# Kernel optimization log

Measured on AMD Instinct MI355X. Metric: run time of the kernel, lower is better.

## Reference

```python
import jax, jax.numpy as jnp
import numpy as np

SIGMA_MIN, SIGMA_MAX = 0.03, 0.35
LAMBDA_GEO = 8.0
COMPAT_SCALE = 0.1
INVALID_W = 0.05
NH, HD = 8, 64
LN_EPS = 1e-5

def _ln(x, g, b):
    m = x.mean(-1, keepdims=True)
    v = ((x - m) ** 2).mean(-1, keepdims=True)
    return (x - m) * jax.lax.rsqrt(v + LN_EPS) * g + b

def setup_inputs() -> dict:
    key = jax.random.key(0)
    ks = jax.random.split(key, 32)
    B, C, H, W = 8, 512, 32, 32
    T, S, D, SIN = 1024, 1024, 512, 512
    s = 0.02
    inp = {
        'front_feat': jax.random.normal(ks[0], (B, C, H, W), jnp.float32),
        'sat_tokens': jax.random.normal(ks[1], (B, S, SIN), jnp.float32),
        'sat_xy': jax.random.uniform(ks[2], (B, S, 2), jnp.float32),
        'front_bev_xy': jax.random.uniform(ks[3], (B, T, 2), jnp.float32),
        'front_bev_valid_mask': jax.random.bernoulli(ks[4], 0.9, (B, T)),
        'front_plucker': jax.random.normal(ks[5], (B, T, 6), jnp.float32),
        'fa_w': jax.random.normal(ks[6], (C, D), jnp.float32) * s,
        'fa_b': jnp.zeros((D,), jnp.float32),
        'fa_g': jnp.ones((D,), jnp.float32),
        'fa_lb': jnp.zeros((D,), jnp.float32),
        'sa_w': jax.random.normal(ks[7], (SIN, D), jnp.float32) * s,
        'sa_b': jnp.zeros((D,), jnp.float32),
        'sa_g': jnp.ones((D,), jnp.float32),
        'sa_lb': jnp.zeros((D,), jnp.float32),
        'q_w': jax.random.normal(ks[8], (D, D), jnp.float32) * s,
        'q_b': jnp.zeros((D,), jnp.float32),
        'k_w': jax.random.normal(ks[9], (D, D), jnp.float32) * s,
        'k_b': jnp.zeros((D,), jnp.float32),
        'v_w': jax.random.normal(ks[10], (D, D), jnp.float32) * s,
        'v_b': jnp.zeros((D,), jnp.float32),
        'pl_w1': jax.random.normal(ks[11], (6, D), jnp.float32) * s,
        'pl_b1': jnp.zeros((D,), jnp.float32),
        'pl_w2': jax.random.normal(ks[12], (D, D), jnp.float32) * s,
        'pl_b2': jnp.zeros((D,), jnp.float32),
        'sig_w': jax.random.normal(ks[13], (D, 1), jnp.float32) * s,
        'sig_b': jnp.zeros((1,), jnp.float32),
        'db_w': jax.random.normal(ks[14], (D, NH), jnp.float32) * s,
        'db_b': jnp.zeros((NH,), jnp.float32),
        'out_w': jax.random.normal(ks[15], (D, C), jnp.float32) * s,
        'out_b': jnp.zeros((C,), jnp.float32),
    }
    return inp

def _forward(front_feat, sat_tokens, sat_xy, front_bev_xy, front_plucker,
             fa_w, fa_b, fa_g, fa_lb, sa_w, sa_b, sa_g, sa_lb,
             q_w, q_b, k_w, k_b, v_w, v_b, pl_w1, pl_b1, pl_w2, pl_b2,
             sig_w, sig_b, db_w, db_b, out_w, out_b, valid_mask):
    B, C, H, W = front_feat.shape
    T = H * W
    D = NH * HD
    front_flat = front_feat.reshape(B, C, T).transpose(0, 2, 1)  # [B,T,C]
    front_embed = _ln(front_flat @ fa_w + fa_b, fa_g, fa_lb)
    pl = jax.nn.silu(front_plucker @ pl_w1 + pl_b1) @ pl_w2 + pl_b2
    context = front_embed + pl
    sat_embed = _ln(sat_tokens @ sa_w + sa_b, sa_g, sa_lb)
    def heads(x):
        return x.reshape(B, -1, NH, HD).transpose(0, 2, 1, 3)  # [B,H,N,d]
    q = heads(front_embed @ q_w + q_b)
    k = heads(sat_embed @ k_w + k_b)
    v = heads(sat_embed @ v_w + v_b)
    compat = jnp.einsum('bhtd,bhsd->bhts', q, k) / jnp.sqrt(jnp.float32(HD))
    compat = COMPAT_SCALE * compat
    sigma = SIGMA_MIN + (SIGMA_MAX - SIGMA_MIN) * jax.nn.sigmoid((context @ sig_w + sig_b)[..., 0])  # [B,T]
    dist2 = ((front_bev_xy[:, :, None, :] - sat_xy[:, None, :, :]) ** 2).sum(-1)  # [B,T,S]
    geo = -LAMBDA_GEO * dist2 / jnp.maximum(sigma[..., None] ** 2, 1e-6)
    sat_logits = compat + geo[:, None]  # [B,H,T,S]
    sat_logits = jnp.where(valid_mask[:, None, :, None], sat_logits, jnp.float32(-10000.0))
    dustbin = (context @ db_w + db_b).transpose(0, 2, 1)[..., None]  # [B,H,T,1]
    logits = jnp.concatenate([sat_logits, dustbin], axis=-1)
    probs = jax.nn.softmax(logits, axis=-1)
    sat_probs, dustbin_prob = probs[..., :-1], probs[..., -1]
    read = jnp.einsum('bhts,bhsd->bhtd', sat_probs, v)
    read = read.transpose(0, 2, 1, 3).reshape(B, T, D)
    read_feat = (read @ out_w + out_b).transpose(0, 2, 1).reshape(B, C, H, W)
    confidence = (1.0 - dustbin_prob).mean(axis=1)  # [B,T]
    conf_feat = confidence.reshape(B, 1, H, W)
    front_feat_out = front_feat + conf_feat * read_feat
    vf = valid_mask.astype(confidence.dtype)
    inv = 1.0 - vf
    invalid_conf = (confidence * inv).sum() / jnp.maximum(inv.sum(), 1.0)
    invalid_conf_loss = invalid_conf * INVALID_W
    return front_feat_out, read_feat, confidence, invalid_conf_loss

def reference(front_feat, sat_tokens, sat_xy, front_bev_xy, front_bev_valid_mask, front_plucker,
              fa_w, fa_b, fa_g, fa_lb, sa_w, sa_b, sa_g, sa_lb,
              q_w, q_b, k_w, k_b, v_w, v_b, pl_w1, pl_b1, pl_w2, pl_b2,
              sig_w, sig_b, db_w, db_b, out_w, out_b):
    return _forward(front_feat, sat_tokens, sat_xy, front_bev_xy, front_plucker,
                    fa_w, fa_b, fa_g, fa_lb, sa_w, sa_b, sa_g, sa_lb,
                    q_w, q_b, k_w, k_b, v_w, v_b, pl_w1, pl_b1, pl_w2, pl_b2,
                    sig_w, sig_b, db_w, db_b, out_w, out_b, front_bev_valid_mask)
```

## Files before the change

### kernel.cpp

```cpp
#include <hip/hip_runtime.h>

typedef unsigned short u16;
typedef __attribute__((ext_vector_type(8))) short short8;
typedef __attribute__((ext_vector_type(4))) float f32x4;

constexpr int B_  = 8;
constexpr int C_  = 512;
constexpr int T_  = 1024;
constexpr int S_  = 1024;
constexpr int D_  = 512;
constexpr int NH_ = 8;
constexpr int BT_ = B_ * T_;
constexpr float INVLN2 = 1.44269504088896340736f;
constexpr float QSCALE2 = 0.0125f * INVLN2;

__device__ __forceinline__ unsigned pack2(float lo, float hi) {
    unsigned r;
    asm("v_cvt_pk_bf16_f32 %0, %1, %2" : "=v"(r) : "v"(lo), "v"(hi));
    return r;
}
__device__ __forceinline__ u16 f2bf(float x) {
    return (u16)pack2(x, x);
}
__device__ __forceinline__ float bf2f(u16 h) {
    union { unsigned u; float f; } v; v.u = ((unsigned)h) << 16;
    return v.f;
}
__device__ __forceinline__ float fexp2(float x) {
    float r;
    asm("v_exp_f32 %0, %1" : "=v"(r) : "v"(x));
    return r;
}
__device__ __forceinline__ float max3f(float a, float b, float c) {
    float r;
    asm("v_max3_f32 %0, %1, %2, %3" : "=v"(r) : "v"(a), "v"(b), "v"(c));
    return r;
}

typedef __attribute__((address_space(3))) unsigned int lds_u32;
typedef const __attribute__((address_space(1))) unsigned int glob_u32;
__device__ __forceinline__ void g2l16(void* l, const void* g) {
    __builtin_amdgcn_global_load_lds((glob_u32*)g, (lds_u32*)l, 16, 0, 0);
}

__device__ __forceinline__ int is_valid(const void* mask, int mode, int idx) {
    if (mode == 0) return ((const int*)mask)[idx] != 0;
    if (mode == 1) return ((const float*)mask)[idx] != 0.0f;
    return ((const unsigned char*)mask)[idx] != 0;
}

__global__ __launch_bounds__(256) void prep_k(
    const float* __restrict__ ff, const float* __restrict__ sat,
    const float* __restrict__ pl,
    const float* a0, const float* a1, const float* a2, const float* a3,
    const float* a4, const float* a5, const float* a6, u16* __restrict__ WT,
    u16* __restrict__ ffb, u16* __restrict__ satb,
    const float* __restrict__ plw1, const float* __restrict__ plb1,
    u16* __restrict__ plh,
    const unsigned* __restrict__ maskw, int* __restrict__ mode,
    float* __restrict__ scal) {
    __shared__ float tile[32][33];
    int blk = blockIdx.x, tid = threadIdx.x;
    if (blk < 4096) {
        int t0 = (blk & 31) * 32, c0 = ((blk >> 5) & 15) * 32, b = blk >> 9;
        int tx = tid & 31, ty = tid >> 5;
        const float* ip = ff + (size_t)b * C_ * T_;
        for (int i = ty; i < 32; i += 8)
            tile[i][tx] = ip[(size_t)(c0 + i) * T_ + t0 + tx];
        __syncthreads();
        u16* op = ffb + (size_t)b * T_ * C_;
        for (int i = ty; i < 32; i += 8)
            op[(size_t)(t0 + i) * C_ + c0 + tx] = f2bf(tile[tx][i]);
    } else if (blk < 5888) {
        int idx = blk - 4096;
        const float* srcs[7] = {a0, a1, a2, a3, a4, a5, a6};
        int z = idx >> 8;
        const float* src = srcs[z];
        u16* d = WT + (size_t)z * 512 * 512;
        int k0 = (idx & 15) * 32, n0 = ((idx >> 4) & 15) * 32;
        int tx = tid & 31, ty = tid >> 5;
        for (int i = ty; i < 32; i += 8)
            tile[i][tx] = src[(size_t)(k0 + i) * 512 + n0 + tx];
        __syncthreads();
        for (int i = ty; i < 32; i += 8)
            d[(size_t)(n0 + i) * 512 + k0 + tx] = f2bf(tile[tx][i]);
    } else if (blk < 7936) {
        int i = (blk - 5888) * 256 + tid;
        const float4* p = (const float4*)(sat + (size_t)i * 8);
        float4 a = p[0], b = p[1];
        uint4 o;
        o.x = pack2(a.x, a.y); o.y = pack2(a.z, a.w);
        o.z = pack2(b.x, b.y); o.w = pack2(b.z, b.w);
        *(uint4*)(satb + (size_t)i * 8) = o;
    } else if (blk < 9984) {
        int m = (blk - 7936) * 4 + (tid >> 6);
        int lane = tid & 63;
        float p6[6];
#pragma unroll
        for (int j = 0; j < 6; ++j) p6[j] = pl[(size_t)m * 6 + j];
        int n0 = lane * 8;
        float acc[8];
#pragma unroll
        for (int e = 0; e < 8; ++e) acc[e] = plb1[n0 + e];
#pragma unroll
        for (int j = 0; j < 6; ++j) {
            float4 wv0 = *(const float4*)(plw1 + j * D_ + n0);
            float4 wv1 = *(const float4*)(plw1 + j * D_ + n0 + 4);
            acc[0] += p6[j] * wv0.x; acc[1] += p6[j] * wv0.y;
            acc[2] += p6[j] * wv0.z; acc[3] += p6[j] * wv0.w;
            acc[4] += p6[j] * wv1.x; acc[5] += p6[j] * wv1.y;
            acc[6] += p6[j] * wv1.z; acc[7] += p6[j] * wv1.w;
        }
        uint4 o;
        float s0 = acc[0] / (1.0f + __expf(-acc[0]));
        float s1 = acc[1] / (1.0f + __expf(-acc[1]));
        float s2 = acc[2] / (1.0f + __expf(-acc[2]));
        float s3 = acc[3] / (1.0f + __expf(-acc[3]));
        float s4 = acc[4] / (1.0f + __expf(-acc[4]));
        float s5 = acc[5] / (1.0f + __expf(-acc[5]));
        float s6 = acc[6] / (1.0f + __expf(-acc[6]));
        float s7 = acc[7] / (1.0f + __expf(-acc[7]));
        o.x = pack2(s0, s1); o.y = pack2(s2, s3);
        o.z = pack2(s4, s5); o.w = pack2(s6, s7);
        *(uint4*)(plh + (size_t)m * D_ + n0) = o;
    } else {
        __shared__ int bad_i, bad_f;
        if (tid == 0) { bad_i = 0; bad_f = 0; }
        __syncthreads();
        for (int i = tid; i < 2048; i += 256) {
            unsigned v = maskw[i];
            if (v > 1u) bad_i = 1;
            if (v != 0u && v != 0x3f800000u) bad_f = 1;
        }
        __syncthreads();
        if (tid == 0) {
            *mode = (!bad_i) ? 0 : ((!bad_f) ? 1 : 2);
            scal[0] = 0.0f; scal[1] = 0.0f;
        }
    }
}

__global__ __launch_bounds__(256) void gmm_k(
    const u16* __restrict__ A0, const u16* __restrict__ A1,
    const u16* __restrict__ A2, const u16* __restrict__ A3,
    const u16* __restrict__ Bt0, const u16* __restrict__ Bt1,
    const u16* __restrict__ Bt2, const u16* __restrict__ Bt3,
    const float* __restrict__ bb0, const float* __restrict__ bb1,
    const float* __restrict__ bb2, const float* __restrict__ bb3,
    void* __restrict__ C0v, void* __restrict__ C1v,
    void* __restrict__ C2v, void* __restrict__ C3v,
    int md0, int md1, int md2, int md3,
    const u16* __restrict__ addend,
    const float* __restrict__ ffp, float* __restrict__ out1p,
    const float* __restrict__ dbpp, const void* __restrict__ maskp,
    const int* __restrict__ modep, float* __restrict__ outcp,
    float* __restrict__ scalp) {
    __shared__ u16 As[2][4096];
    __shared__ u16 Bs[2][4096];
    __shared__ float confL[128];
    int jid = blockIdx.x >> 8;
    int L = blockIdx.x & 255;
    const u16* A    = (jid == 0) ? A0 : (jid == 1) ? A1 : (jid == 2) ? A2 : A3;
    const u16* Bt   = (jid == 0) ? Bt0 : (jid == 1) ? Bt1 : (jid == 2) ? Bt2 : Bt3;
    const float* bias = (jid == 0) ? bb0 : (jid == 1) ? bb1 : (jid == 2) ? bb2 : bb3;
    void* Cv        = (jid == 0) ? C0v : (jid == 1) ? C1v : (jid == 2) ? C2v : C3v;
    int mode        = (jid == 0) ? md0 : (jid == 1) ? md1 : (jid == 2) ? md2 : md3;

    int tid = threadIdx.x, w = tid >> 6, l = tid & 63;
    int lr = l & 15, g = l >> 4;
    int W = (L & 7) * 32 + (L >> 3);
    int m0 = (W >> 2) * 128, n0 = (W & 3) * 128;
    int wr = w >> 1, wc = w & 1;
    int prm = g ^ ((lr >> 1) & 3);

    f32x4 acc[4][4] = {};

    auto stage = [&](int buf, int k0) {
#pragma unroll
        for (int j = 0; j < 2; ++j) {
            int i = tid + 256 * j;
            int row = i >> 2, gg = (i & 3) ^ ((i >> 3) & 3);
            g2l16((char*)As[buf] + (size_t)i * 16,
                  A + (size_t)(m0 + row) * 512 + k0 + gg * 8);
        }
#pragma unroll
        for (int j = 0; j < 2; ++j) {
            int i = tid + 256 * j;
            int col = i >> 2, gg = (i & 3) ^ ((i >> 3) & 3);
            g2l16((char*)Bs[buf] + (size_t)i * 16,
                  Bt + (size_t)(n0 + col) * 512 + k0 + gg * 8);
        }
    };

    stage(0, 0);

    if (mode == 4 && tid < 128) {
        int row = m0 + tid;
        const float* dr = dbpp + (size_t)row * NH_;
        float s = 0;
#pragma unroll
        for (int h = 0; h < 8; ++h) s += dr[h];
        float cf = 1.0f - s * 0.125f;
        confL[tid] = cf;
        if ((W & 3) == 0) {
            outcp[row] = cf;
            int md = *modep;
            float invd = is_valid(maskp, md, row) ? 0.0f : 1.0f;
            float a = cf * invd, bsum = invd;
            for (int o = 32; o; o >>= 1) {
                a += __shfl_down(a, o);
                bsum += __shfl_down(bsum, o);
            }
            if ((tid & 63) == 0) {
                atomicAdd(&scalp[0], a);
                atomicAdd(&scalp[1], bsum);
            }
        }
    }

    __syncthreads();
    int cur = 0;
    for (int t = 0; t < 16; ++t) {
        if (t < 15) stage(cur ^ 1, (t + 1) * 32);
        const char* Ab = (const char*)As[cur];
        const char* Bb = (const char*)Bs[cur];
        short8 af[4], bf[4];
#pragma unroll
        for (int m = 0; m < 4; ++m)
            af[m] = *(const short8*)(Ab + ((wr * 64 + m * 16 + lr) * 4 + prm) * 16);
#pragma unroll
        for (int n = 0; n < 4; ++n)
            bf[n] = *(const short8*)(Bb + ((wc * 64 + n * 16 + lr) * 4 + prm) * 16);
        __builtin_amdgcn_s_setprio(1);
#pragma unroll
        for (int m = 0; m < 4; ++m)
#pragma unroll
            for (int n = 0; n < 4; ++n)
                acc[m][n] = __builtin_amdgcn_mfma_f32_16x16x32_bf16(
                    af[m], bf[n], acc[m][n], 0, 0, 0);
        __builtin_amdgcn_s_setprio(0);
        __syncthreads();
        cur ^= 1;
    }

    float bs[4];
#pragma unroll
    for (int n = 0; n < 4; ++n) bs[n] = bias[n0 + wc * 64 + n * 16 + lr];

#pragma unroll
    for (int m = 0; m < 4; ++m) {
#pragma unroll
        for (int n = 0; n < 4; ++n) {
            int R0  = m0 + wr * 64 + m * 16 + 4 * g;
            int col = n0 + wc * 64 + n * 16 + lr;
            if (mode == 3) {
                int bbx = R0 >> 10, ss = R0 & 1023, hh = col >> 6, dd = col & 63;
                uint2 pk;
                pk.x = pack2(acc[m][n][0] + bs[n], acc[m][n][1] + bs[n]);
                pk.y = pack2(acc[m][n][2] + bs[n], acc[m][n][3] + bs[n]);
                u16* dst = (u16*)Cv + ((size_t)(bbx * 8 + hh) * 64 + dd) * 1024 + ss;
                *(uint2*)dst = pk;
            } else if (mode == 4) {
                int bbx = R0 >> 10, t0p = R0 & 1023;
                size_t base = (size_t)bbx * C_ * T_ + (size_t)col * T_ + t0p;
                float4 rf;
                rf.x = acc[m][n][0] + bs[n]; rf.y = acc[m][n][1] + bs[n];
                rf.z = acc[m][n][2] + bs[n]; rf.w = acc[m][n][3] + bs[n];
                float4 ffv = *(const float4*)(ffp + base);
                float4 cfv = *(const float4*)&confL[R0 - m0];
                float4 o0v;
                o0v.x = ffv.x + cfv.x * rf.x; o0v.y = ffv.y + cfv.y * rf.y;
                o0v.z = ffv.z + cfv.z * rf.z; o0v.w = ffv.w + cfv.w * rf.w;
                *(float4*)(out1p + base) = rf;
                *(float4*)((float*)Cv + base) = o0v;
            } else {
#pragma unroll
                for (int j = 0; j < 4; ++j) {
                    int row = R0 + j;
                    float v = acc[m][n][j] + bs[n];
                    if (mode == 1) v *= QSCALE2;
                    if (mode == 2) v += bf2f(addend[(size_t)row * 512 + col]);
                    ((u16*)Cv)[(size_t)row * 512 + col] = f2bf(v);
                }
            }
        }
    }
}

__global__ __launch_bounds__(256) void ln2_k(
    const u16* __restrict__ X0, const float* __restrict__ g0,
    const float* __restrict__ b0, u16* __restrict__ O0,
    const u16* __restrict__ X1, const float* __restrict__ g1,
    const float* __restrict__ b1, u16* __restrict__ O1) {
    int sel = blockIdx.x >> 13;
    int row = blockIdx.x & 8191;
    const u16* X = sel ? X1 : X0;
    const float* gw = sel ? g1 : g0;
    const float* bw = sel ? b1 : b0;
    u16* out = sel ? O1 : O0;
    int tid = threadIdx.x;
    const unsigned* xr = (const unsigned*)(X + (size_t)row * D_);
    unsigned u = xr[tid];
    float x0 = bf2f((u16)(u & 0xffff)), x1 = bf2f((u16)(u >> 16));
    float s = x0 + x1, sq = x0 * x0 + x1 * x1;
    __shared__ float rs[4], rq[4];
    for (int o = 32; o; o >>= 1) { s += __shfl_down(s, o); sq += __shfl_down(sq, o); }
    int wid = tid >> 6, lane = tid & 63;
    if (lane == 0) { rs[wid] = s; rq[wid] = sq; }
    __syncthreads();
    if (tid == 0) {
        float ts = 0, tq = 0;
        for (int w = 0; w < 4; ++w) { ts += rs[w]; tq += rq[w]; }
        rs[0] = ts; rq[0] = tq;
    }
    __syncthreads();
    float mean = rs[0] * (1.0f / D_);
    float var  = rq[0] * (1.0f / D_) - mean * mean;
    float r = rsqrtf(var + 1e-5f);
    float2 g2 = *(const float2*)(gw + 2 * tid);
    float2 b2 = *(const float2*)(bw + 2 * tid);
    float y0 = (x0 - mean) * r * g2.x + b2.x;
    float y1 = (x1 - mean) * r * g2.y + b2.y;
    ((unsigned*)(out + (size_t)row * D_))[tid] = pack2(y0, y1);
}

__global__ __launch_bounds__(256) void head_k(const u16* __restrict__ ctx,
        const float* __restrict__ sw, const float* __restrict__ sbb,
        const float* __restrict__ dw, const float* __restrict__ dbb,
        float* __restrict__ sig, float* __restrict__ dbo) {
    int w = threadIdx.x >> 6, lane = threadIdx.x & 63;
    int row = blockIdx.x * 4 + w;
    const u16* xr = ctx + (size_t)row * D_;
    short8 xv = *(const short8*)(xr + lane * 8);
    float xs[8];
#pragma unroll
    for (int i = 0; i < 8; ++i) xs[i] = bf2f((u16)xv[i]);
    float4 wa = *(const float4*)(sw + lane * 8);
    float4 wb = *(const float4*)(sw + lane * 8 + 4);
    float sacc = xs[0] * wa.x + xs[1] * wa.y + xs[2] * wa.z + xs[3] * wa.w +
                 xs[4] * wb.x + xs[5] * wb.y + xs[6] * wb.z + xs[7] * wb.w;
    float d_[8] = {};
    const float* dr = dw + (size_t)lane * 8 * NH_;
#pragma unroll
    for (int i = 0; i < 8; ++i)
#pragma unroll
        for (int hh = 0; hh < 8; ++hh) d_[hh] += xs[i] * dr[i * NH_ + hh];
    for (int o = 32; o; o >>= 1) {
        sacc += __shfl_down(sacc, o);
#pragma unroll
        for (int hh = 0; hh < 8; ++hh) d_[hh] += __shfl_down(d_[hh], o);
    }
    if (lane == 0) {
        float z = sacc + sbb[0];
        sig[row] = 0.03f + 0.32f / (1.0f + __expf(-z));
        float* dd = dbo + (size_t)row * NH_;
#pragma unroll
        for (int hh = 0; hh < 8; ++hh) dd[hh] = d_[hh] + dbb[hh];
    }
}

__global__ __launch_bounds__(512) void attn_k(
    const u16* __restrict__ Q, const u16* __restrict__ K,
    const u16* __restrict__ Vt, const float* __restrict__ sig,
    const float* __restrict__ dbl, const float* __restrict__ bev,
    const float* __restrict__ sxy, const void* __restrict__ mask,
    const int* __restrict__ mode, u16* __restrict__ OUT,
    float* __restrict__ dbp) {
    int L = blockIdx.x;
    int W = (L & 7) * 64 + (L >> 3);
    int b = W >> 6, h = (W >> 3) & 7, tblk = W & 7;
    int tid = threadIdx.x, w = tid >> 6, l = tid & 63;
    int lr = l & 15, g = l >> 4;
    int p8 = lr & 7;

    __shared__ u16 Kbuf[2][4096];
    __shared__ u16 Vbuf[2][4096];
    __shared__ float2 SXY[1024];
    __shared__ float  SZ[1024];

    const float2* xp = (const float2*)(sxy + (size_t)b * S_ * 2);
#pragma unroll
    for (int j = 0; j < 2; ++j) {
        int idx = tid + 512 * j;
        float2 v = xp[idx];
        SXY[idx] = make_float2(-2.0f * v.x, -2.0f * v.y);
        SZ[idx] = v.x * v.x + v.y * v.y;
    }

    int trow = b * T_ + tblk * 128 + w * 16 + lr;
    float s_ = sig[trow];
    float bx = bev[(size_t)trow * 2], by = bev[(size_t)trow * 2 + 1];
    float dbv2 = dbl[(size_t)trow * NH_ + h] * INVLN2;
    int md = *mode;
    bool vld = is_valid(mask, md, trow) != 0;
    float grow  = vld ? (-11.5415603271117f / fmaxf(s_ * s_, 1e-6f)) : 0.0f;
    float Abase = vld ? grow * (bx * bx + by * by) : -10000.0f;
    float AbaseM = Abase - dbv2;
    float mshift = 0.0f;

    const u16* qp = Q + (size_t)trow * 512 + h * 64 + g * 8;
    short8 q0 = *(const short8*)qp;
    short8 q1 = *(const short8*)(qp + 32);
    if (!vld) { q0 = short8{}; q1 = short8{}; }

    short8 ones;
#pragma unroll
    for (int e = 0; e < 8; ++e) ones[e] = (short)0x3F80;

    const u16* Kp = K + (size_t)b * S_ * 512 + h * 64;
    const u16* Vp = Vt + (size_t)(b * 8 + h) * 64 * 1024;

    int srow = tid >> 3;
    int gprm = (tid & 7) ^ (srow & 7);
    int sK = ((srow >> 5) & 1) * 32 + ((srow >> 2) & 3) * 8 +
             ((srow >> 4) & 1) * 4 + (srow & 3);

    auto stageKV = [&](int buf, int s0) {
        g2l16((char*)Kbuf[buf] + (size_t)tid * 16,
              Kp + (size_t)(s0 + sK) * 512 + gprm * 8);
        g2l16((char*)Vbuf[buf] + (size_t)tid * 16,
              Vp + (size_t)srow * 1024 + s0 + gprm * 8);
    };

    f32x4 o0 = {}, o1 = {}, o2 = {}, o3 = {};
    f32x4 o4 = {1.0f, 1.0f, 1.0f, 1.0f};

    stageKV(0, 0);
    __syncthreads();
    int cur = 0;
    for (int c = 0; c < 16; ++c) {
        int s0c = c * 64;
        if (c < 15) stageKV(cur ^ 1, s0c + 64);

        const char* Kc = (const char*)Kbuf[cur];
        const char* Vc = (const char*)Vbuf[cur];

        f32x4 p[4];
        f32x4 z4 = {};
        __builtin_amdgcn_s_setprio(1);
#pragma unroll
        for (int sub = 0; sub < 4; ++sub) {
            int krow = sub * 16 + lr;
            short8 kf0 = *(const short8*)(Kc + (krow * 8 + (g ^ p8)) * 16);
            short8 kf1 = *(const short8*)(Kc + (krow * 8 + ((4 + g) ^ p8)) * 16);
            p[sub] = __builtin_amdgcn_mfma_f32_16x16x32_bf16(kf0, q0, z4, 0, 0, 0);
            p[sub] = __builtin_amdgcn_mfma_f32_16x16x32_bf16(kf1, q1, p[sub], 0, 0, 0);
        }
        __builtin_amdgcn_s_setprio(0);

        float lg[16];
#pragma unroll
        for (int sub = 0; sub < 4; ++sub) {
            int sl = s0c + ((sub & 2) << 4) + 8 * g + ((sub & 1) << 2);
            float4 xy01 = *(const float4*)&SXY[sl];
            float4 xy23 = *(const float4*)&SXY[sl + 2];
            float4 zz   = *(const float4*)&SZ[sl];
            float X[4] = {xy01.x, xy01.z, xy23.x, xy23.z};
            float Y[4] = {xy01.y, xy01.w, xy23.y, xy23.w};
            float Z[4] = {zz.x, zz.y, zz.z, zz.w};
#pragma unroll
            for (int i2 = 0; i2 < 4; ++i2) {
                float wg = fmaf(bx, X[i2], fmaf(by, Y[i2], Z[i2]));
                lg[sub * 4 + i2] = fmaf(grow, wg, p[sub][i2] + AbaseM);
            }
        }
        float c0 = max3f(lg[0], lg[1], lg[2]);
        float c1 = max3f(lg[3], lg[4], lg[5]);
        float c2 = max3f(lg[6], lg[7], lg[8]);
        float c3 = max3f(lg[9], lg[10], lg[11]);
        float c4 = max3f(lg[12], lg[13], lg[14]);
        float cl = fmaxf(max3f(c0, c1, c2), max3f(c3, c4, lg[15]));

        if (!__all(cl <= 11.5f)) {
            cl = fmaxf(cl, __shfl_xor(cl, 16));
            cl = fmaxf(cl, __shfl_xor(cl, 32));
            float dm = fmaxf(cl, 0.0f);
            float scl = fexp2(-dm);
            o0 *= scl; o1 *= scl; o2 *= scl; o3 *= scl; o4 *= scl;
            AbaseM -= dm;
            mshift -= dm;
#pragma unroll
            for (int r = 0; r < 16; ++r) lg[r] -= dm;
        }
        float pe[16];
#pragma unroll
        for (int r = 0; r < 16; ++r) pe[r] = fexp2(lg[r]);

        union { uint4 u; short8 s8; } pf0, pf1;
        pf0.u.x = pack2(pe[0], pe[1]);  pf0.u.y = pack2(pe[2], pe[3]);
        pf0.u.z = pack2(pe[4], pe[5]);  pf0.u.w = pack2(pe[6], pe[7]);
        pf1.u.x = pack2(pe[8], pe[9]);  pf1.u.y = pack2(pe[10], pe[11]);
        pf1.u.z = pack2(pe[12], pe[13]); pf1.u.w = pack2(pe[14], pe[15]);

        __builtin_amdgcn_s_setprio(1);
        short8 vf;
#pragma unroll
        for (int dt = 0; dt < 4; ++dt) {
            int vrow = dt * 16 + lr;
            f32x4* oo = (dt == 0) ? &o0 : (dt == 1) ? &o1 : (dt == 2) ? &o2 : &o3;
            vf = *(const short8*)(Vc + (vrow * 8 + (g ^ p8)) * 16);
            *oo = __builtin_amdgcn_mfma_f32_16x16x32_bf16(vf, pf0.s8, *oo, 0, 0, 0);
            vf = *(const short8*)(Vc + (vrow * 8 + ((4 + g) ^ p8)) * 16);
            *oo = __builtin_amdgcn_mfma_f32_16x16x32_bf16(vf, pf1.s8, *oo, 0, 0, 0);
        }
        o4 = __builtin_amdgcn_mfma_f32_16x16x32_bf16(ones, pf0.s8, o4, 0, 0, 0);
        o4 = __builtin_amdgcn_mfma_f32_16x16x32_bf16(ones, pf1.s8, o4, 0, 0, 0);
        __builtin_amdgcn_s_setprio(0);

        __syncthreads();
        cur ^= 1;
    }

    float inv = 1.0f / o4[0];
    u16* ob = OUT + (size_t)trow * 512 + h * 64;
    {
        uint2 pk;
        pk.x = pack2(o0[0] * inv, o0[1] * inv); pk.y = pack2(o0[2] * inv, o0[3] * inv);
        *(uint2*)(ob + 0 * 16 + 4 * g) = pk;
        pk.x = pack2(o1[0] * inv, o1[1] * inv); pk.y = pack2(o1[2] * inv, o1[3] * inv);
        *(uint2*)(ob + 1 * 16 + 4 * g) = pk;
        pk.x = pack2(o2[0] * inv, o2[1] * inv); pk.y = pack2(o2[2] * inv, o2[3] * inv);
        *(uint2*)(ob + 2 * 16 + 4 * g) = pk;
        pk.x = pack2(o3[0] * inv, o3[1] * inv); pk.y = pack2(o3[2] * inv, o3[3] * inv);
        *(uint2*)(ob + 3 * 16 + 4 * g) = pk;
    }
    if (g == 0) dbp[(size_t)trow * NH_ + h] = fexp2(mshift) * inv;
}

__global__ void loss_k(const float* __restrict__ scal, float* __restrict__ out) {
    out[0] = scal[0] / fmaxf(scal[1], 1.0f) * 0.05f;
}

extern "C" void kernel_launch(void* const* d_in, const int* in_sizes, int n_in,
                              void* d_out, int out_size, void* d_ws, size_t ws_size,
                              hipStream_t stream) {
    const float* front_feat = (const float*)d_in[0];
    const float* sat_tokens = (const float*)d_in[1];
    const float* sat_xy     = (const float*)d_in[2];
    const float* bev_xy     = (const float*)d_in[3];
    const void*  mask       = d_in[4];
    const float* plucker    = (const float*)d_in[5];
    const float* fa_w = (const float*)d_in[6];
    const float* fa_b = (const float*)d_in[7];
    const float* fa_g = (const float*)d_in[8];
    const float* fa_lb = (const float*)d_in[9];
    const float* sa_w = (const float*)d_in[10];
    const float* sa_b = (const float*)d_in[11];
    const float* sa_g = (const float*)d_in[12];
    const float* sa_lb = (const float*)d_in[13];
    const float* q_w = (const float*)d_in[14];
    const float* q_b = (const float*)d_in[15];
    const float* k_w = (const float*)d_in[16];
    const float* k_b = (const float*)d_in[17];
    const float* v_w = (const float*)d_in[18];
    const float* v_b = (const float*)d_in[19];
    const float* pl_w1 = (const float*)d_in[20];
    const float* pl_b1 = (const float*)d_in[21];
    const float* pl_w2 = (const float*)d_in[22];
    const float* pl_b2 = (const float*)d_in[23];
    const float* sig_w = (const float*)d_in[24];
    const float* sig_b = (const float*)d_in[25];
    const float* db_w = (const float*)d_in[26];
    const float* db_b = (const float*)d_in[27];
    const float* out_w = (const float*)d_in[28];
    const float* out_b = (const float*)d_in[29];

    char* w8 = (char*)d_ws;
    u16* H0 = (u16*)(w8);
    u16* H1 = (u16*)(w8 + 8388608ull * 1);
    u16* H2 = (u16*)(w8 + 8388608ull * 2);
    u16* H3 = (u16*)(w8 + 8388608ull * 3);
    u16* H4 = (u16*)(w8 + 8388608ull * 4);
    u16* H5 = (u16*)(w8 + 8388608ull * 5);
    u16* H6 = (u16*)(w8 + 8388608ull * 6);
    u16* WT = (u16*)(w8 + 8388608ull * 7);
    char* sm = w8 + 8388608ull * 7 + 3670016ull;
    float* w_sigma = (float*)sm;
    float* w_db    = w_sigma + BT_;
    float* w_dbp   = w_db + (size_t)BT_ * NH_;
    float* w_scal  = w_dbp + (size_t)BT_ * NH_;
    int*   w_mode  = (int*)(w_scal + 2);

    u16* Wfa = WT;                 u16* Wpl2 = WT + 262144ull * 1;
    u16* Wq  = WT + 262144ull * 2; u16* Wsa  = WT + 262144ull * 3;
    u16* Wk  = WT + 262144ull * 4; u16* Wv   = WT + 262144ull * 5;
    u16* Wo  = WT + 262144ull * 6;

    float* out0 = (float*)d_out;
    float* out1 = out0 + (size_t)B_ * C_ * T_;
    float* outc = out1 + (size_t)B_ * C_ * T_;
    float* outl = outc + (size_t)B_ * T_;

    dim3 blk(256);

    prep_k<<<dim3(9985), blk, 0, stream>>>(
        front_feat, sat_tokens, plucker,
        fa_w, pl_w2, q_w, sa_w, k_w, v_w, out_w, WT,
        H0, H5, pl_w1, pl_b1, H2,
        (const unsigned*)mask, w_mode, w_scal);
    gmm_k<<<dim3(512), blk, 0, stream>>>(
        H0, H5, nullptr, nullptr,
        Wfa, Wsa, nullptr, nullptr,
        fa_b, sa_b, nullptr, nullptr,
        H6, H4, nullptr, nullptr,
        0, 0, 0, 0,
        nullptr, nullptr, nullptr,
        nullptr, nullptr, nullptr, nullptr, nullptr);
    ln2_k<<<dim3(16384), blk, 0, stream>>>(H6, fa_g, fa_lb, H1,
                                           H4, sa_g, sa_lb, H3);
    gmm_k<<<dim3(1024), blk, 0, stream>>>(
        H1, H2, H3, H3,
        Wq, Wpl2, Wk, Wv,
        q_b, pl_b2, k_b, v_b,
        H5, H6, H0, H4,
        1, 2, 0, 3,
        H1, nullptr, nullptr,
        nullptr, nullptr, nullptr, nullptr, nullptr);
    head_k<<<dim3(BT_ / 4), blk, 0, stream>>>(H6, sig_w, sig_b, db_w, db_b,
                                              w_sigma, w_db);
    attn_k<<<dim3(512), dim3(512), 0, stream>>>(
        H5, H0, H4, w_sigma, w_db, bev_xy, sat_xy, mask, w_mode, H2, w_dbp);
    gmm_k<<<dim3(256), blk, 0, stream>>>(
        H2, nullptr, nullptr, nullptr,
        Wo, nullptr, nullptr, nullptr,
        out_b, nullptr, nullptr, nullptr,
        out0, nullptr, nullptr, nullptr,
        4, 0, 0, 0,
        nullptr, front_feat, out1,
        w_dbp, mask, w_mode, outc, w_scal);
    loss_k<<<1, 1, 0, stream>>>(w_scal, outl);
}
```

Before: 163.3 us.

## Triple-buffer GEMM K-loop and use partial vmcnt waits in attention

The fused GEMM kernel moves from double to triple-buffered LDS staging. Each iteration issues the load two tiles ahead, then waits with an explicit s_waitcnt vmcnt(8) so only the current tile's async global-to-LDS loads must finish before the barrier. The attention kernel also uses a partial vmcnt wait (2) after issuing the next K/V chunk, so that prefetch stays in flight during compute instead of being drained by __syncthreads. This is meant to hide global-load latency better, at the cost of more LDS per block (possible occupancy loss) and reliance on correct hand-counted vmcnt values.

```diff
diff --git a/kernel.cpp b/kernel.cpp
--- a/kernel.cpp
+++ b/kernel.cpp
@@ -36,6 +36,12 @@
     asm("v_max3_f32 %0, %1, %2, %3" : "=v"(r) : "v"(a), "v"(b), "v"(c));
     return r;
 }
+
+#define GWAITBAR(N) do { \
+    asm volatile("s_waitcnt vmcnt(" #N ") lgkmcnt(0)" ::: "memory"); \
+    __builtin_amdgcn_sched_barrier(0); \
+    __builtin_amdgcn_s_barrier(); \
+    __builtin_amdgcn_sched_barrier(0); } while (0)
 
 typedef __attribute__((address_space(3))) unsigned int lds_u32;
 typedef const __attribute__((address_space(1))) unsigned int glob_u32;
@@ -155,8 +161,8 @@
     const float* __restrict__ dbpp, const void* __restrict__ maskp,
     const int* __restrict__ modep, float* __restrict__ outcp,
     float* __restrict__ scalp) {
-    __shared__ u16 As[2][4096];
-    __shared__ u16 Bs[2][4096];
+    __shared__ u16 As[3][4096];
+    __shared__ u16 Bs[3][4096];
     __shared__ float confL[128];
     int jid = blockIdx.x >> 8;
     int L = blockIdx.x & 255;
@@ -174,25 +180,6 @@
     int prm = g ^ ((lr >> 1) & 3);
 
     f32x4 acc[4][4] = {};
-
-    auto stage = [&](int buf, int k0) {
-#pragma unroll
-        for (int j = 0; j < 2; ++j) {
-            int i = tid + 256 * j;
-            int row = i >> 2, gg = (i & 3) ^ ((i >> 3) & 3);
-            g2l16((char*)As[buf] + (size_t)i * 16,
-                  A + (size_t)(m0 + row) * 512 + k0 + gg * 8);
-        }
-#pragma unroll
-        for (int j = 0; j < 2; ++j) {
-            int i = tid + 256 * j;
-            int col = i >> 2, gg = (i & 3) ^ ((i >> 3) & 3);
-            g2l16((char*)Bs[buf] + (size_t)i * 16,
-                  Bt + (size_t)(n0 + col) * 512 + k0 + gg * 8);
-        }
-    };
-
-    stage(0, 0);
 
     if (mode == 4 && tid < 128) {
         int row = m0 + tid;
@@ -218,12 +205,26 @@
         }
     }
 
-    __syncthreads();
-    int cur = 0;
-    for (int t = 0; t < 16; ++t) {
-        if (t < 15) stage(cur ^ 1, (t + 1) * 32);
-        const char* Ab = (const char*)As[cur];
-        const char* Bb = (const char*)Bs[cur];
+    auto stage = [&](int buf, int k0) {
+#pragma unroll
+        for (int j = 0; j < 2; ++j) {
+            int i = tid + 256 * j;
+            int row = i >> 2, gg = (i & 3) ^ ((i >> 3) & 3);
+            g2l16((char*)As[buf] + (size_t)i * 16,
+                  A + (size_t)(m0 + row) * 512 + k0 + gg * 8);
+        }
+#pragma unroll
+        for (int j = 0; j < 2; ++j) {
+            int i = tid + 256 * j;
+            int col = i >> 2, gg = (i & 3) ^ ((i >> 3) & 3);
+            g2l16((char*)Bs[buf] + (size_t)i * 16,
+                  Bt + (size_t)(n0 + col) * 512 + k0 + gg * 8);
+        }
+    };
+
+    auto compute = [&](int bi) {
+        const char* Ab = (const char*)As[bi];
+        const char* Bb = (const char*)Bs[bi];
         short8 af[4], bf[4];
 #pragma unroll
         for (int m = 0; m < 4; ++m)
@@ -239,9 +240,20 @@
                 acc[m][n] = __builtin_amdgcn_mfma_f32_16x16x32_bf16(
                     af[m], bf[n], acc[m][n], 0, 0, 0);
         __builtin_amdgcn_s_setprio(0);
-        __syncthreads();
-        cur ^= 1;
-    }
+    };
+
+    stage(0, 0);
+    stage(1, 32);
+    for (int t = 0; t < 14; ++t) {
+        stage((t + 2) % 3, (t + 2) * 32);
+        GWAITBAR(8);
+        compute(t % 3);
+        __builtin_amdgcn_s_barrier();
+    }
+    GWAITBAR(4);
+    compute(2);
+    GWAITBAR(0);
+    compute(0);
 
     float bs[4];
 #pragma unroll
@@ -426,11 +438,15 @@
     f32x4 o4 = {1.0f, 1.0f, 1.0f, 1.0f};
 
     stageKV(0, 0);
-    __syncthreads();
     int cur = 0;
     for (int c = 0; c < 16; ++c) {
         int s0c = c * 64;
-        if (c < 15) stageKV(cur ^ 1, s0c + 64);
+        if (c < 15) {
+            stageKV(cur ^ 1, s0c + 64);
+            GWAITBAR(2);
+        } else {
+            GWAITBAR(0);
+        }
 
         const char* Kc = (const char*)Kbuf[cur];
         const char* Vc = (const char*)Vbuf[cur];
@@ -507,7 +523,7 @@
         o4 = __builtin_amdgcn_mfma_f32_16x16x32_bf16(ones, pf1.s8, o4, 0, 0, 0);
         __builtin_amdgcn_s_setprio(0);
 
-        __syncthreads();
+        __builtin_amdgcn_s_barrier();
         cur ^= 1;
     }
 
```

Result: faster. 159.3 us (-2.5%).
